# Performance work log

Hardware: AMD Instinct MI355X
Metric: run time of the kernel (lower is better)

The kernel has to match this reference:

```python
import jax, jax.numpy as jnp
import numpy as np

NUM_MEL = 80
STACK_FRAMES = 4   # encoder.embed.right_context + 1
STRIDE = 4         # encoder.embed.subsampling_rate
N_SUB = 1          # n_subsequent
NCB = 1            # num_codebooks
EMB_DIM = 16
NUM_EMB = 8192
ENC_DIM = 512
B, T = 16, 2048
T_ENC = (T - STACK_FRAMES) // STRIDE + 1  # 512
EPS_LN = 1e-6


def setup_inputs() -> dict:
    key = jax.random.key(0)
    k = jax.random.split(key, 6)
    feats = jax.random.normal(k[0], (B, T, NUM_MEL), dtype=jnp.float32)
    feats_lengths = jax.random.randint(k[1], (B,), T // 2, T + 1, dtype=jnp.int32)
    encoder_out = jax.random.normal(k[2], (B, T_ENC, ENC_DIM), dtype=jnp.float32)
    in_dim = NUM_MEL * STRIDE
    lim = float(np.sqrt(6.0 / (in_dim + EMB_DIM * NCB)))  # xavier-uniform
    projection = jax.random.uniform(k[3], (in_dim, EMB_DIM * NCB), jnp.float32, -lim, lim)
    emb = jax.random.normal(k[4], (NUM_EMB, NCB, EMB_DIM), dtype=jnp.float32)
    embeddings = emb / (jnp.linalg.norm(emb, axis=-1, keepdims=True) + 1e-8)
    top_n_out = 0.02 * jax.random.normal(k[5], (N_SUB, NCB, ENC_DIM, NUM_EMB), dtype=jnp.float32)
    return {"feats": feats, "feats_lengths": feats_lengths, "encoder_out": encoder_out,
            "projection": projection, "embeddings": embeddings, "top_n_out": top_n_out}


def _stack_features(feats, lens):
    b, t, f = feats.shape
    n = (t - STACK_FRAMES) // STRIDE + 1
    idx = jnp.arange(n)[:, None] * STRIDE + jnp.arange(STACK_FRAMES)[None, :]  # [n, S]
    stack = feats[:, idx, :].reshape(b, n, STACK_FRAMES * f)                   # [B, n, S*F]
    mask = jnp.arange(t)[None, :] < lens[:, None]                              # [B, T]
    sub_mask = jnp.all(mask[:, idx], axis=-1)                                  # [B, n]
    mean = stack.mean(-1, keepdims=True)
    var = stack.var(-1, keepdims=True)
    stack = (stack - mean) * jax.lax.rsqrt(var + EPS_LN)  # LayerNorm, no affine
    return stack, sub_mask


def _nearest_idx(stack, projection, embeddings):
    x = stack @ projection                                         # [B, n, ncb*E]
    x = x / (jnp.linalg.norm(x, axis=-1, keepdims=True) + 1e-8)
    b, n, _ = x.shape
    v, ncb, e = embeddings.shape
    xf = x.reshape(b * n, ncb, e)
    dots = jnp.einsum('nce,vce->ncv', xf, embeddings)              # [N, ncb, V]
    x2 = jnp.sum(xf * xf, -1, keepdims=True)                       # [N, ncb, 1]
    e2 = jnp.sum(embeddings * embeddings, -1).T[None]              # [1, ncb, V]
    dist = x2 - 2.0 * dots + e2
    codes = jnp.argmin(dist, axis=-1)                              # [N, ncb]
    return codes.reshape(b, n, ncb)


def _forward(feats, feats_lengths, encoder_out, projection, embeddings, top_n_out):
    stack, stack_mask = _stack_features(feats, feats_lengths)
    target = _nearest_idx(stack, projection, embeddings)           # [B, n, ncb]
    tq = stack_mask.shape[1]
    # unfold(n_subsequent=1) -> [B, Tq, ns, ncb]
    target = target[:, :tq, None, :]
    # encoder output mask (subsampled lengths)
    t_enc = encoder_out.shape[1]
    out_mask = jnp.arange(t_enc)[None, :] < (feats_lengths // STRIDE)[:, None]
    logits = jnp.einsum('btd,scdv->bsctv', encoder_out, top_n_out)  # [B, ns, ncb, T', V]
    logits = logits[:, :, :, :tq, :][:, :, :, :-1, :]               # frames 0..Tq-2
    target = target[:, 1:]                                          # targets 1..Tq-1
    masks = (out_mask[:, :tq] & stack_mask)[:, 1:]                  # [B, Tq-1] bool
    mf = masks.astype(logits.dtype)
    logp = jax.nn.log_softmax(logits, axis=-1)
    tgt_bsct = jnp.transpose(target, (0, 2, 3, 1))                  # [B, ns, ncb, Tq-1]
    nll = -jnp.take_along_axis(logp, tgt_bsct[..., None], axis=-1)[..., 0]
    mfull = jnp.broadcast_to(mf[:, None, None, :], nll.shape)
    loss = (nll * mfull).sum() / mfull.sum()
    num_codes = mf.sum() * NCB
    pred = jnp.argmax(logits, axis=-1)                              # [B, ns, ncb, Tq-1]
    corr = (pred == tgt_bsct).astype(logits.dtype)
    codes_acc = (corr * mfull).sum() / num_codes
    masked_tgt = target * masks[:, :, None, None].astype(target.dtype)
    presence = jnp.zeros((NUM_EMB,), jnp.int32).at[masked_tgt.reshape(-1)].set(1)
    uniq_num_codes = presence.sum().astype(jnp.float32)
    return loss, codes_acc, num_codes, uniq_num_codes


def reference(feats, feats_lengths, encoder_out, projection, embeddings, top_n_out):
    return _forward(feats, feats_lengths, encoder_out, projection, embeddings, top_n_out)
```

## Files before the change

kernel.cpp:

```cpp
#include <hip/hip_runtime.h>
#include <math.h>

typedef __attribute__((ext_vector_type(4))) float f32x4;
typedef __attribute__((ext_vector_type(8))) short bf16x8;

#define NB 16
#define NT 2048
#define NMEL 80
#define NPOS 512
#define EDIM 16
#define NEMB 8192
#define ENCD 512
#define MROWS (NB*511)
#define MPAD 8192
#define NVT 64

__device__ __forceinline__ void gl_lds16(const void* gsrc, void* lds) {
    __builtin_amdgcn_global_load_lds(
        (const __attribute__((address_space(1))) unsigned int*)gsrc,
        (__attribute__((address_space(3))) unsigned int*)lds,
        16, 0, 0);
}

__global__ __launch_bounds__(256) void prep_kernel(
    const float* __restrict__ feats, const float* __restrict__ proj,
    const float* __restrict__ emb, const float* __restrict__ enc,
    const float* __restrict__ tno,
    int* __restrict__ codes, int* __restrict__ presence,
    unsigned char* __restrict__ encF8, unsigned char* __restrict__ tnoF8)
{
    __shared__ float tileT[32][33];
    const int bid = blockIdx.x;
    const int tid = threadIdx.x;

    if (bid < 512) {
        const int lane = tid & 63;
        const int wave = tid >> 6;
        const int gbase = bid * 16 + wave * 4;
        if (bid < 32) presence[bid * 256 + tid] = 0;

        float yn[4][EDIM];
        #pragma unroll
        for (int pi = 0; pi < 4; ++pi) {
            const int g = gbase + pi;
            const int b = g >> 9;
            const int i = g & 511;
            float xv[5];
            float s = 0.f, sq = 0.f;
            #pragma unroll
            for (int qq = 0; qq < 5; ++qq) {
                const int d = lane + 64 * qq;
                const int j = d / 80, k = d - j * 80;
                const float v = feats[((b * NT) + (i * 4 + j)) * NMEL + k];
                xv[qq] = v; s += v; sq += v * v;
            }
            for (int m = 1; m < 64; m <<= 1) { s += __shfl_xor(s, m); sq += __shfl_xor(sq, m); }
            const float mean = s * (1.0f / 320.0f);
            const float var  = sq * (1.0f / 320.0f) - mean * mean;
            const float rstd = rsqrtf(var + 1e-6f);
            float acc[EDIM];
            #pragma unroll
            for (int e = 0; e < EDIM; ++e) acc[e] = 0.f;
            #pragma unroll
            for (int qq = 0; qq < 5; ++qq) {
                const int d = lane + 64 * qq;
                const float xn = (xv[qq] - mean) * rstd;
                #pragma unroll
                for (int e = 0; e < EDIM; ++e) acc[e] += xn * proj[d * EDIM + e];
            }
            for (int m = 1; m < 64; m <<= 1) {
                #pragma unroll
                for (int e = 0; e < EDIM; ++e) acc[e] += __shfl_xor(acc[e], m);
            }
            float nsq = 0.f;
            #pragma unroll
            for (int e = 0; e < EDIM; ++e) nsq += acc[e] * acc[e];
            const float inv = 1.0f / (sqrtf(nsq) + 1e-8f);
            #pragma unroll
            for (int e = 0; e < EDIM; ++e) yn[pi][e] = acc[e] * inv;
        }

        float mind[4]; int mini[4];
        #pragma unroll
        for (int pi = 0; pi < 4; ++pi) { mind[pi] = INFINITY; mini[pi] = 0x7fffffff; }

        #pragma unroll 2
        for (int i = 0; i < 128; ++i) {
            const int v = i * 64 + lane;
            const float* ep = &emb[(size_t)v * EDIM];
            const float4 e0 = *(const float4*)&ep[0];
            const float4 e1 = *(const float4*)&ep[4];
            const float4 e2v = *(const float4*)&ep[8];
            const float4 e3 = *(const float4*)&ep[12];
            const float e2 = e0.x*e0.x + e0.y*e0.y + e0.z*e0.z + e0.w*e0.w
                           + e1.x*e1.x + e1.y*e1.y + e1.z*e1.z + e1.w*e1.w
                           + e2v.x*e2v.x + e2v.y*e2v.y + e2v.z*e2v.z + e2v.w*e2v.w
                           + e3.x*e3.x + e3.y*e3.y + e3.z*e3.z + e3.w*e3.w;
            const float h2 = 0.5f * e2;
            #pragma unroll
            for (int pi = 0; pi < 4; ++pi) {
                const float dot = yn[pi][0]*e0.x + yn[pi][1]*e0.y + yn[pi][2]*e0.z + yn[pi][3]*e0.w
                                + yn[pi][4]*e1.x + yn[pi][5]*e1.y + yn[pi][6]*e1.z + yn[pi][7]*e1.w
                                + yn[pi][8]*e2v.x + yn[pi][9]*e2v.y + yn[pi][10]*e2v.z + yn[pi][11]*e2v.w
                                + yn[pi][12]*e3.x + yn[pi][13]*e3.y + yn[pi][14]*e3.z + yn[pi][15]*e3.w;
                const float sc = h2 - dot;
                if (sc < mind[pi]) { mind[pi] = sc; mini[pi] = v; }
            }
        }
        for (int m = 1; m < 64; m <<= 1) {
            #pragma unroll
            for (int pi = 0; pi < 4; ++pi) {
                const float ov = __shfl_xor(mind[pi], m);
                const int   oi = __shfl_xor(mini[pi], m);
                if (ov < mind[pi] || (ov == mind[pi] && oi < mini[pi])) { mind[pi] = ov; mini[pi] = oi; }
            }
        }
        if (lane == 0) {
            #pragma unroll
            for (int pi = 0; pi < 4; ++pi) codes[gbase + pi] = mini[pi];
        }
    } else if (bid < 1024) {
        const int bid2 = bid - 512;
        const int lane = tid & 63;
        #pragma unroll
        for (int pass = 0; pass < 4; ++pass) {
            const int m = bid2 * 16 + pass * 4 + (tid >> 6);
            const int d = lane * 8;
            uint2 o = make_uint2(0u, 0u);
            if (m < MROWS) {
                const int b = m / 511, t = m - b * 511;
                const float4 f0 = *(const float4*)&enc[((size_t)(b * 512 + t)) * ENCD + d];
                const float4 f1 = *(const float4*)&enc[((size_t)(b * 512 + t)) * ENCD + d + 4];
                int w0 = __builtin_amdgcn_cvt_pk_fp8_f32(f0.x, f0.y, 0, false);
                w0     = __builtin_amdgcn_cvt_pk_fp8_f32(f0.z, f0.w, w0, true);
                int w1 = __builtin_amdgcn_cvt_pk_fp8_f32(f1.x, f1.y, 0, false);
                w1     = __builtin_amdgcn_cvt_pk_fp8_f32(f1.z, f1.w, w1, true);
                o.x = (unsigned)w0; o.y = (unsigned)w1;
            }
            *(uint2*)&encF8[(size_t)m * ENCD + d] = o;
        }
    } else {
        const int bid2 = bid - 1024;
        const int tx = tid & 31, ty = tid >> 5;
        const int np = tid >> 3, kc = tid & 7;
        #pragma unroll
        for (int it = 0; it < 4; ++it) {
            const int tile = bid2 * 4 + it;
            const int n0 = (tile & 255) * 32;
            const int k0 = (tile >> 8) * 32;
            __syncthreads();
            #pragma unroll
            for (int i = 0; i < 4; ++i)
                tileT[ty + 8 * i][tx] = tno[(size_t)(k0 + ty + 8 * i) * NEMB + n0 + tx];
            __syncthreads();
            const float t0 = 16.0f * tileT[kc * 4 + 0][np];
            const float t1 = 16.0f * tileT[kc * 4 + 1][np];
            const float t2 = 16.0f * tileT[kc * 4 + 2][np];
            const float t3 = 16.0f * tileT[kc * 4 + 3][np];
            int w = __builtin_amdgcn_cvt_pk_fp8_f32(t0, t1, 0, false);
            w     = __builtin_amdgcn_cvt_pk_fp8_f32(t2, t3, w, true);
            ((unsigned*)tnoF8)[(size_t)(n0 + np) * (ENCD / 4) + (k0 >> 2) + kc] = (unsigned)w;
        }
    }
}

__global__ __launch_bounds__(256, 3) void logits_mfma(
    const unsigned char* __restrict__ encF8, const unsigned char* __restrict__ tnoF8,
    const int* __restrict__ codes,
    float* __restrict__ pm, float* __restrict__ ps, int* __restrict__ pidx,
    float* __restrict__ tgtlog)
{
    __shared__ __align__(16) unsigned char As3[3][128 * 64];
    __shared__ __align__(16) unsigned char Bs3[3][128 * 64];
    __shared__ float redM[2][128];
    __shared__ float redS[2][128];
    __shared__ int   redI[2][128];

    const int tid  = threadIdx.x;
    const int lane = tid & 63;
    const int wave = tid >> 6;
    const int wr = wave >> 1, wc = wave & 1;

    const int bid = blockIdx.x;
    const int xcd = bid & 7;
    const int idx = bid >> 3;
    const int mt  = xcd * 8 + (idx & 7);
    const int vt  = idx >> 3;
    const int m0 = mt * 128, n0 = vt * 128;

    const int rb   = lane >> 2;
    const int gcB  = ((lane & 3) ^ ((lane >> 3) & 3)) * 16;
    const size_t abase0 = (size_t)(m0 + wave * 32 + rb) * ENCD + gcB;
    const size_t bbase0 = (size_t)(n0 + wave * 32 + rb) * ENCD + gcB;

#define STAGE(t, buf)                                                                        \
    {                                                                                        \
        const int k0s = (t) * 64;                                                            \
        gl_lds16(encF8 + abase0 + k0s,              &As3[buf][(wave * 32) * 64]);            \
        gl_lds16(tnoF8 + bbase0 + k0s,              &Bs3[buf][(wave * 32) * 64]);            \
        gl_lds16(encF8 + abase0 + 16 * ENCD + k0s,  &As3[buf][(wave * 32 + 16) * 64]);       \
        gl_lds16(tnoF8 + bbase0 + 16 * ENCD + k0s,  &Bs3[buf][(wave * 32 + 16) * 64]);       \
    }

    f32x4 acc[4][4];
    #pragma unroll
    for (int i = 0; i < 4; ++i)
        #pragma unroll
        for (int j = 0; j < 4; ++j)
            acc[i][j] = (f32x4){0.f, 0.f, 0.f, 0.f};

    const int l15 = lane & 15, q = lane >> 4;
    const int rsw = (l15 >> 1) & 3;

    STAGE(0, 0);
    STAGE(1, 1);

    #pragma unroll
    for (int t = 0; t < 8; ++t) {
        if (t < 7) { asm volatile("s_waitcnt vmcnt(4)" ::: "memory"); }
        else       { asm volatile("s_waitcnt vmcnt(0)" ::: "memory"); }
        __builtin_amdgcn_s_barrier();
        __builtin_amdgcn_sched_barrier(0);
        if (t + 2 < 8) {
            const int nb = (t + 2) % 3;
            STAGE(t + 2, nb);
        }
        const unsigned char* Ab = As3[t % 3];
        const unsigned char* Bb = Bs3[t % 3];
        #pragma unroll
        for (int ks = 0; ks < 2; ++ks) {
            const int co = ((ks * 2 + (q >> 1)) ^ rsw) * 16 + (q & 1) * 8;
            long a[4], b[4];
            #pragma unroll
            for (int mi = 0; mi < 4; ++mi)
                a[mi] = *(const long*)&Ab[(wr * 64 + mi * 16 + l15) * 64 + co];
            #pragma unroll
            for (int ni = 0; ni < 4; ++ni)
                b[ni] = *(const long*)&Bb[(wc * 64 + ni * 16 + l15) * 64 + co];
            __builtin_amdgcn_s_setprio(1);
            #pragma unroll
            for (int mi = 0; mi < 4; ++mi)
                #pragma unroll
                for (int ni = 0; ni < 4; ++ni)
                    acc[mi][ni] = __builtin_amdgcn_mfma_f32_16x16x32_fp8_fp8(a[mi], b[ni], acc[mi][ni], 0, 0, 0);
            __builtin_amdgcn_s_setprio(0);
        }
    }
#undef STAGE

    #pragma unroll
    for (int mi = 0; mi < 4; ++mi)
        #pragma unroll
        for (int ni = 0; ni < 4; ++ni)
            acc[mi][ni] *= 0.0625f;

    #pragma unroll
    for (int mi = 0; mi < 4; ++mi) {
        #pragma unroll
        for (int r = 0; r < 4; ++r) {
            const int rl = wr * 64 + mi * 16 + q * 4 + r;
            float lm = -INFINITY; int li = 0;
            #pragma unroll
            for (int ni = 0; ni < 4; ++ni) {
                const float v = acc[mi][ni][r];
                const int col = wc * 64 + ni * 16 + l15;
                if (v > lm) { lm = v; li = col; }
            }
            #pragma unroll
            for (int mk = 8; mk >= 1; mk >>= 1) {
                const float ov = __shfl_xor(lm, mk);
                const int   oi = __shfl_xor(li, mk);
                if (ov > lm || (ov == lm && oi < li)) { lm = ov; li = oi; }
            }
            float le = 0.f;
            #pragma unroll
            for (int ni = 0; ni < 4; ++ni) le += __expf(acc[mi][ni][r] - lm);
            #pragma unroll
            for (int mk = 8; mk >= 1; mk >>= 1) le += __shfl_xor(le, mk);

            if (l15 == 0) { redM[wc][rl] = lm; redS[wc][rl] = le; redI[wc][rl] = li; }

            const int mg = m0 + rl;
            if (mg < MROWS) {
                const int bb = mg / 511, tt = mg - bb * 511;
                const int tv = codes[bb * NPOS + tt + 1];
                const int rel = tv - n0 - wc * 64;
                #pragma unroll
                for (int ni = 0; ni < 4; ++ni) {
                    if (rel >= ni * 16 && rel < ni * 16 + 16 && (rel & 15) == l15)
                        tgtlog[mg] = acc[mi][ni][r];
                }
            }
        }
    }
    __syncthreads();
    if (tid < 128) {
        const int rl = tid;
        const int mg = m0 + rl;
        if (mg < MROWS) {
            const float mA = redM[0][rl], mB = redM[1][rl];
            const int   iA = redI[0][rl], iB = redI[1][rl];
            float gm; int gi;
            if (mB > mA || (mB == mA && iB + 64 < iA)) { gm = mB; gi = 64 + iB; } else { gm = mA; gi = iA; }
            const float S = redS[0][rl] * __expf(mA - gm) + redS[1][rl] * __expf(mB - gm);
            pm[(size_t)vt * MPAD + mg]   = gm;
            ps[(size_t)vt * MPAD + mg]   = S;
            pidx[(size_t)vt * MPAD + mg] = n0 + gi;
        }
    }
}

__global__ __launch_bounds__(256) void combine_kernel(
    const float* __restrict__ pm, const float* __restrict__ ps,
    const int* __restrict__ pidx, const float* __restrict__ tgtlog,
    const int* __restrict__ codes, const int* __restrict__ lens,
    float* __restrict__ rnll, float* __restrict__ rcorr, float* __restrict__ rmf,
    int* __restrict__ presence)
{
    const int g = blockIdx.x * 256 + threadIdx.x;
    if (g >= MROWS) return;
    float gm = -INFINITY; int gi = 0;
    #pragma unroll 8
    for (int nt = 0; nt < NVT; ++nt) {
        const float v = pm[(size_t)nt * MPAD + g];
        if (v > gm) { gm = v; gi = pidx[(size_t)nt * MPAD + g]; }
    }
    float S = 0.f;
    #pragma unroll 8
    for (int nt = 0; nt < NVT; ++nt) S += ps[(size_t)nt * MPAD + g] * __expf(pm[(size_t)nt * MPAD + g] - gm);
    const float lse = gm + logf(S);
    const int b = g / 511, t = g - b * 511;
    const int tv = codes[b * NPOS + t + 1];
    const float nll = lse - tgtlog[g];
    const int L = lens[b];
    const int s = t + 1;
    const bool mf = (s < (L / 4)) && (4 * s + 3 < L);
    rnll[g]  = mf ? nll : 0.f;
    rcorr[g] = (mf && gi == tv) ? 1.f : 0.f;
    rmf[g]   = mf ? 1.f : 0.f;
    if (mf) presence[tv] = 1;
}

__global__ __launch_bounds__(256) void finalize_kernel(
    const float* __restrict__ rnll, const float* __restrict__ rcorr,
    const float* __restrict__ rmf, const int* __restrict__ presence,
    float* __restrict__ out)
{
    __shared__ float sh0[256], sh1[256], sh2[256];
    __shared__ int shp[256];
    const int tid = threadIdx.x;
    float sn = 0.f, sc = 0.f, sm = 0.f; int pp = 0;
    for (int g = tid; g < MROWS; g += 256) { sn += rnll[g]; sc += rcorr[g]; sm += rmf[g]; }
    for (int v = tid; v < NEMB; v += 256) pp += presence[v];
    sh0[tid] = sn; sh1[tid] = sc; sh2[tid] = sm; shp[tid] = pp;
    __syncthreads();
    for (int s = 128; s > 0; s >>= 1) {
        if (tid < s) { sh0[tid] += sh0[tid + s]; sh1[tid] += sh1[tid + s]; sh2[tid] += sh2[tid + s]; shp[tid] += shp[tid + s]; }
        __syncthreads();
    }
    if (tid == 0) {
        const float Sm = sh2[0];
        out[0] = sh0[0] / Sm;
        out[1] = sh1[0] / Sm;
        out[2] = Sm;
        out[3] = (float)shp[0];
    }
}

extern "C" void kernel_launch(void* const* d_in, const int* in_sizes, int n_in,
                              void* d_out, int out_size, void* d_ws, size_t ws_size,
                              hipStream_t stream) {
    const float* feats = (const float*)d_in[0];
    const int*   lens  = (const int*)d_in[1];
    const float* enc   = (const float*)d_in[2];
    const float* proj  = (const float*)d_in[3];
    const float* emb   = (const float*)d_in[4];
    const float* tno   = (const float*)d_in[5];
    float* out = (float*)d_out;

    int* codes          = (int*)d_ws;
    int* presence       = codes + MPAD;
    float* pm           = (float*)(presence + MPAD);
    float* ps           = pm + (size_t)NVT * MPAD;
    int* pidx           = (int*)(ps + (size_t)NVT * MPAD);
    float* tgtlog       = (float*)(pidx + (size_t)NVT * MPAD);
    float* rnll         = tgtlog + MPAD;
    float* rcorr        = rnll + MPAD;
    float* rmf          = rcorr + MPAD;
    unsigned char* encF8 = (unsigned char*)(rmf + MPAD);
    unsigned char* tnoF8 = encF8 + (size_t)MPAD * ENCD;

    hipLaunchKernelGGL(prep_kernel, dim3(2048), dim3(256), 0, stream,
                       feats, proj, emb, enc, tno, codes, presence, encF8, tnoF8);
    hipLaunchKernelGGL(logits_mfma, dim3(64 * 64), dim3(256), 0, stream, encF8, tnoF8, codes, pm, ps, pidx, tgtlog);
    hipLaunchKernelGGL(combine_kernel, dim3((MROWS + 255) / 256), dim3(256), 0, stream,
                       pm, ps, pidx, tgtlog, codes, lens, rnll, rcorr, rmf, presence);
    hipLaunchKernelGGL(finalize_kernel, dim3(1), dim3(256), 0, stream, rnll, rcorr, rmf, presence, out);
}
```

Before: 245.2 us.

## Split nearest-codebook search across four vocab chunks with a merge kernel

```diff
diff --git a/kernel.cpp b/kernel.cpp
--- a/kernel.cpp
+++ b/kernel.cpp
@@ -2,7 +2,6 @@
 #include <math.h>
 
 typedef __attribute__((ext_vector_type(4))) float f32x4;
-typedef __attribute__((ext_vector_type(8))) short bf16x8;
 
 #define NB 16
 #define NT 2048
@@ -26,17 +25,20 @@
     const float* __restrict__ feats, const float* __restrict__ proj,
     const float* __restrict__ emb, const float* __restrict__ enc,
     const float* __restrict__ tno,
-    int* __restrict__ codes, int* __restrict__ presence,
+    float* __restrict__ pscore, int* __restrict__ pcidx,
+    int* __restrict__ presence,
     unsigned char* __restrict__ encF8, unsigned char* __restrict__ tnoF8)
 {
     __shared__ float tileT[32][33];
     const int bid = blockIdx.x;
     const int tid = threadIdx.x;
 
-    if (bid < 512) {
+    if (bid < 2048) {
+        const int pgrp  = bid >> 2;
+        const int chunk = bid & 3;
         const int lane = tid & 63;
         const int wave = tid >> 6;
-        const int gbase = bid * 16 + wave * 4;
+        const int gbase = pgrp * 16 + wave * 4;
         if (bid < 32) presence[bid * 256 + tid] = 0;
 
         float yn[4][EDIM];
@@ -85,8 +87,8 @@
         for (int pi = 0; pi < 4; ++pi) { mind[pi] = INFINITY; mini[pi] = 0x7fffffff; }
 
         #pragma unroll 2
-        for (int i = 0; i < 128; ++i) {
-            const int v = i * 64 + lane;
+        for (int i = 0; i < 32; ++i) {
+            const int v = chunk * 2048 + i * 64 + lane;
             const float* ep = &emb[(size_t)v * EDIM];
             const float4 e0 = *(const float4*)&ep[0];
             const float4 e1 = *(const float4*)&ep[4];
@@ -117,10 +119,13 @@
         }
         if (lane == 0) {
             #pragma unroll
-            for (int pi = 0; pi < 4; ++pi) codes[gbase + pi] = mini[pi];
-        }
-    } else if (bid < 1024) {
-        const int bid2 = bid - 512;
+            for (int pi = 0; pi < 4; ++pi) {
+                pscore[chunk * MPAD + gbase + pi] = mind[pi];
+                pcidx [chunk * MPAD + gbase + pi] = mini[pi];
+            }
+        }
+    } else if (bid < 2560) {
+        const int bid2 = bid - 2048;
         const int lane = tid & 63;
         #pragma unroll
         for (int pass = 0; pass < 4; ++pass) {
@@ -140,7 +145,7 @@
             *(uint2*)&encF8[(size_t)m * ENCD + d] = o;
         }
     } else {
-        const int bid2 = bid - 1024;
+        const int bid2 = bid - 2560;
         const int tx = tid & 31, ty = tid >> 5;
         const int np = tid >> 3, kc = tid & 7;
         #pragma unroll
@@ -162,6 +167,21 @@
             ((unsigned*)tnoF8)[(size_t)(n0 + np) * (ENCD / 4) + (k0 >> 2) + kc] = (unsigned)w;
         }
     }
+}
+
+__global__ __launch_bounds__(256) void codes_merge(
+    const float* __restrict__ pscore, const int* __restrict__ pcidx,
+    int* __restrict__ codes)
+{
+    const int g = blockIdx.x * 256 + threadIdx.x;
+    float m = INFINITY; int mi = 0x7fffffff;
+    #pragma unroll
+    for (int c = 0; c < 4; ++c) {
+        const float s = pscore[c * MPAD + g];
+        const int  ix = pcidx [c * MPAD + g];
+        if (s < m || (s == m && ix < mi)) { m = s; mi = ix; }
+    }
+    codes[g] = mi;
 }
 
 __global__ __launch_bounds__(256, 3) void logits_mfma(
@@ -387,11 +407,14 @@
     float* rnll         = tgtlog + MPAD;
     float* rcorr        = rnll + MPAD;
     float* rmf          = rcorr + MPAD;
-    unsigned char* encF8 = (unsigned char*)(rmf + MPAD);
+    float* pscore       = rmf + MPAD;
+    int*   pcidx        = (int*)(pscore + 4 * MPAD);
+    unsigned char* encF8 = (unsigned char*)(pcidx + 4 * MPAD);
     unsigned char* tnoF8 = encF8 + (size_t)MPAD * ENCD;
 
-    hipLaunchKernelGGL(prep_kernel, dim3(2048), dim3(256), 0, stream,
-                       feats, proj, emb, enc, tno, codes, presence, encF8, tnoF8);
+    hipLaunchKernelGGL(prep_kernel, dim3(3584), dim3(256), 0, stream,
+                       feats, proj, emb, enc, tno, pscore, pcidx, presence, encF8, tnoF8);
+    hipLaunchKernelGGL(codes_merge, dim3(32), dim3(256), 0, stream, pscore, pcidx, codes);
     hipLaunchKernelGGL(logits_mfma, dim3(64 * 64), dim3(256), 0, stream, encF8, tnoF8, codes, pm, ps, pidx, tgtlog);
     hipLaunchKernelGGL(combine_kernel, dim3((MROWS + 255) / 256), dim3(256), 0, stream,
                        pm, ps, pidx, tgtlog, codes, lens, rnll, rcorr, rmf, presence);
```

Measured after the change: 267.7 us. +9.2%, slower.
